# Performance work log

Measured on AMD Instinct MI355X. Metric: run time of the kernel, lower is better.

The kernel has to match this reference:

```python
import jax, jax.numpy as jnp
import numpy as np

B, N, HIDDEN, IN_DIM = 4, 1024, 64, 6


def setup_inputs() -> dict:
    key = jax.random.key(0)
    ks = jax.random.split(key, 8)
    pos = jax.random.normal(ks[0], (B, N, 3), dtype=jnp.float32)
    vel = jax.random.normal(ks[1], (B, N, 3), dtype=jnp.float32)
    # edge MLP params (Linear stores W as [out,in] in torch; we use [in,out])
    s1 = 1.0 / np.sqrt(IN_DIM)
    s2 = 1.0 / np.sqrt(HIDDEN)
    W1 = jax.random.uniform(ks[2], (IN_DIM, HIDDEN), jnp.float32, -s1, s1)
    b1 = jax.random.uniform(ks[3], (HIDDEN,), jnp.float32, -s1, s1)
    W2 = jax.random.uniform(ks[4], (HIDDEN, HIDDEN), jnp.float32, -s2, s2)
    b2 = jax.random.uniform(ks[5], (HIDDEN,), jnp.float32, -s2, s2)
    W3 = jax.random.uniform(ks[6], (HIDDEN, 3), jnp.float32, -s2, s2)
    b3 = jax.random.uniform(ks[7], (3,), jnp.float32, -s2, s2)
    return {"pos": pos, "vel": vel, "W1": W1, "b1": b1, "W2": W2, "b2": b2, "W3": W3, "b3": b3}


def reference(pos, vel, W1, b1, W2, b2, W3, b3):
    # all-pairs differences: r_ij[b,i,j] = pos[b,j] - pos[b,i]   [B,N,N,3]
    r_ij = pos[:, None, :, :] - pos[:, :, None, :]
    v_ij = vel[:, None, :, :] - vel[:, :, None, :]
    edge_inputs = jnp.concatenate([r_ij, v_ij], axis=-1)  # [B,N,N,6]
    h = jax.nn.relu(jnp.einsum('bijk,kh->bijh', edge_inputs, W1) + b1)
    h = jax.nn.relu(jnp.einsum('bijh,hg->bijg', h, W2) + b2)
    f_ij = jnp.einsum('bijg,go->bijo', h, W3) + b3  # [B,N,N,3]
    # antisymmetrize over (i,j); diagonal becomes exactly 0
    f_sym = (f_ij - jnp.swapaxes(f_ij, 1, 2)) * 0.5
    acc = jnp.sum(f_sym, axis=2)  # [B,N,3]
    return acc
```

## Files before the change

### kernel.cpp

```cpp
#include <hip/hip_runtime.h>

#define NB   4
#define NPTS 1024
#define HID  64
#define TPB  64
#define UPB  2080

typedef float f32x4 __attribute__((ext_vector_type(4)));
typedef float f32x2 __attribute__((ext_vector_type(2)));
typedef short bf16x8 __attribute__((ext_vector_type(8)));
typedef unsigned int u32;
typedef unsigned short u16;

__device__ inline u16 f2bf(float x) {
    union { float f; unsigned u; } v; v.f = x;
    return (u16)((v.u + 0x7FFFu + ((v.u >> 16) & 1u)) >> 16);
}
__device__ inline u32 cvt_pk_bf16(float lo, float hi) {
    u32 r; asm("v_cvt_pk_bf16_f32 %0, %1, %2" : "=v"(r) : "v"(lo), "v"(hi)); return r;
}
__device__ inline u32 pk_relu2(u32 a) {
    u32 r; asm("v_pk_max_i16 %0, %1, 0" : "=v"(r) : "v"(a)); return r;
}

__global__ __launch_bounds__(256) void precompute(
    const float* __restrict__ pos, const float* __restrict__ vel,
    const float* __restrict__ W1, const float* __restrict__ W2,
    float* __restrict__ P, u16* __restrict__ W2T) {
    if (blockIdx.x == NB * NPTS / 4) {
        for (int e = threadIdx.x; e < HID * HID; e += 256) {
            const int ch = e >> 6, k = e & 63;
            W2T[e] = f2bf(W2[k * HID + ch]);
        }
        return;
    }
    const int t   = blockIdx.x * 256 + threadIdx.x;
    const int row = t >> 6;
    const int k   = t & 63;
    const float* pp = pos + row * 3;
    const float* vv = vel + row * 3;
    float acc = 0.f;
    #pragma unroll
    for (int c = 0; c < 3; ++c) acc = fmaf(pp[c], W1[c * HID + k], acc);
    #pragma unroll
    for (int c = 0; c < 3; ++c) acc = fmaf(vv[c], W1[(3 + c) * HID + k], acc);
    P[row * HID + k] = acc;
}

__device__ inline void emit_tile(const f32x4 Ht[4], float sgn, int rowbase,
                                 const float* __restrict__ W3,
                                 float* __restrict__ F, int c, int g) {
    #pragma unroll
    for (int r = 0; r < 4; ++r) {
        float f0 = 0.f, f1 = 0.f, f2 = 0.f;
        #pragma unroll
        for (int n = 0; n < 4; ++n) {
            const int ch = n * 16 + c;
            const float h = Ht[n][r];
            f0 = fmaf(h, W3[ch * 3 + 0], f0);
            f1 = fmaf(h, W3[ch * 3 + 1], f1);
            f2 = fmaf(h, W3[ch * 3 + 2], f2);
        }
        #pragma unroll
        for (int off = 1; off < 16; off <<= 1) {
            f0 += __shfl_xor(f0, off, 64);
            f1 += __shfl_xor(f1, off, 64);
            f2 += __shfl_xor(f2, off, 64);
        }
        if (c < 3) {
            const float v = (c == 0) ? f0 : ((c == 1) ? f1 : f2);
            atomicAdd(&F[(size_t)(rowbase + g * 4 + r) * 3 + c], sgn * v);
        }
    }
}

__global__ __launch_bounds__(128, 3) void inet_pair(
    const float* __restrict__ P,  const float* __restrict__ b1,
    const u16* __restrict__ W2T,  const float* __restrict__ b2,
    const float* __restrict__ W3, float* __restrict__ F) {
    __shared__ __align__(16) u16 sBf[512 * 8];

    const int tid = threadIdx.x;
    for (int s = tid; s < 512; s += 128) {
        const int f = s >> 6, l = s & 63;
        const int n = f & 3, kk = f >> 2, cc = l & 15, gg = l >> 4;
        ((uint4*)sBf)[s] = *(const uint4*)(W2T + (size_t)(n * 16 + cc) * HID + kk * 32 + gg * 8);
    }
    __syncthreads();

    const int lane = tid & 63;
    const int c    = lane & 15;
    const int g    = lane >> 4;

    const int unit = blockIdx.x * 2 + (tid >> 6);
    const int b    = unit / UPB;
    const int p    = unit - b * UPB;
    int I = (int)((129.0f - sqrtf((float)(16641 - 8 * p))) * 0.5f);
    while (I * (129 - I) / 2 > p) --I;
    while ((I + 1) * (128 - I) / 2 <= p) ++I;
    const int J = I + (p - I * (129 - I) / 2);
    const bool diag = (I == J);

    const float* Pb   = P + (size_t)b * NPTS * HID;
    const int    koff = g * 8;

    union V4 { f32x4 v; f32x2 p[2]; };

    f32x2 PJp[8], PJm[8];
    {
        const float* base = Pb + (size_t)(J * 16 + c) * HID + koff;
        V4 v0, v1, v2, v3, u0, u1, u2, u3;
        v0.v = *(const f32x4*)(base);
        v1.v = *(const f32x4*)(base + 4);
        v2.v = *(const f32x4*)(base + 32);
        v3.v = *(const f32x4*)(base + 36);
        u0.v = *(const f32x4*)(b1 + koff);
        u1.v = *(const f32x4*)(b1 + koff + 4);
        u2.v = *(const f32x4*)(b1 + koff + 32);
        u3.v = *(const f32x4*)(b1 + koff + 36);
        PJp[0] = v0.p[0] + u0.p[0];  PJm[0] = v0.p[0] - u0.p[0];
        PJp[1] = v0.p[1] + u0.p[1];  PJm[1] = v0.p[1] - u0.p[1];
        PJp[2] = v1.p[0] + u1.p[0];  PJm[2] = v1.p[0] - u1.p[0];
        PJp[3] = v1.p[1] + u1.p[1];  PJm[3] = v1.p[1] - u1.p[1];
        PJp[4] = v2.p[0] + u2.p[0];  PJm[4] = v2.p[0] - u2.p[0];
        PJp[5] = v2.p[1] + u2.p[1];  PJm[5] = v2.p[1] - u2.p[1];
        PJp[6] = v3.p[0] + u3.p[0];  PJm[6] = v3.p[0] - u3.p[0];
        PJp[7] = v3.p[1] + u3.p[1];  PJm[7] = v3.p[1] - u3.p[1];
    }
    float b2v[4];
    #pragma unroll
    for (int n = 0; n < 4; ++n) b2v[n] = b2[n * 16 + c];

    f32x4 Hi[4], Hj[4];
    #pragma unroll
    for (int n = 0; n < 4; ++n) {
        Hi[n] = (f32x4){0.f, 0.f, 0.f, 0.f};
        Hj[n] = (f32x4){0.f, 0.f, 0.f, 0.f};
    }

    const float* Pi0 = Pb + (size_t)(I * 16) * HID + koff;

    for (int i1 = 0; i1 < 4; ++i1) {
        const float selm = (g == i1) ? 1.0f : 0.0f;
        #pragma unroll
        for (int i2 = 0; i2 < 4; ++i2) {
            const float* pib = Pi0 + (size_t)(i1 * 4 + i2) * HID;
            V4 w0, w1, w2, w3;
            w0.v = *(const f32x4*)(pib);
            w1.v = *(const f32x4*)(pib + 4);
            w2.v = *(const f32x4*)(pib + 32);
            w3.v = *(const f32x4*)(pib + 36);
            f32x2 pi2[8];
            pi2[0] = w0.p[0]; pi2[1] = w0.p[1]; pi2[2] = w1.p[0]; pi2[3] = w1.p[1];
            pi2[4] = w2.p[0]; pi2[5] = w2.p[1]; pi2[6] = w3.p[0]; pi2[7] = w3.p[1];

            union { bf16x8 v; u32 u[4]; } ap[2], am[2];
            #pragma unroll
            for (int kk = 0; kk < 2; ++kk)
                #pragma unroll
                for (int d = 0; d < 4; ++d) {
                    f32x2 tp = PJp[kk * 4 + d] - pi2[kk * 4 + d];
                    f32x2 tm = pi2[kk * 4 + d] - PJm[kk * 4 + d];
                    ap[kk].u[d] = pk_relu2(cvt_pk_bf16(tp.x, tp.y));
                    am[kk].u[d] = pk_relu2(cvt_pk_bf16(tm.x, tm.y));
                }

            #pragma unroll
            for (int n = 0; n < 4; ++n) {
                const bf16x8 B0 = ((const bf16x8*)sBf)[n * 64 + lane];
                const bf16x8 B1 = ((const bf16x8*)sBf)[(4 + n) * 64 + lane];
                const f32x4 Ci = {b2v[n], b2v[n], b2v[n], b2v[n]};
                f32x4 Cp = __builtin_amdgcn_mfma_f32_16x16x32_bf16(ap[0].v, B0, Ci, 0, 0, 0);
                Cp       = __builtin_amdgcn_mfma_f32_16x16x32_bf16(ap[1].v, B1, Cp, 0, 0, 0);
                f32x4 Cm = __builtin_amdgcn_mfma_f32_16x16x32_bf16(am[0].v, B0, Ci, 0, 0, 0);
                Cm       = __builtin_amdgcn_mfma_f32_16x16x32_bf16(am[1].v, B1, Cm, 0, 0, 0);
                V4 dd;
                dd.p[0] = (f32x2){fmaxf(Cp[0], 0.f) - fmaxf(Cm[0], 0.f),
                                  fmaxf(Cp[1], 0.f) - fmaxf(Cm[1], 0.f)};
                dd.p[1] = (f32x2){fmaxf(Cp[2], 0.f) - fmaxf(Cm[2], 0.f),
                                  fmaxf(Cp[3], 0.f) - fmaxf(Cm[3], 0.f)};
                if (!diag) {
                    Hj[n][0] += dd.v[0]; Hj[n][1] += dd.v[1];
                    Hj[n][2] += dd.v[2]; Hj[n][3] += dd.v[3];
                }
                f32x2 q = dd.p[0] + dd.p[1];
                float s = q.x + q.y;
                s += __shfl_xor(s, 16, 64);
                s += __shfl_xor(s, 32, 64);
                Hi[n][i2] = fmaf(selm, s, Hi[n][i2]);
            }
        }
    }

    const int rowbase = b * NPTS;
    emit_tile(Hi, 0.5f, rowbase + I * 16, W3, F, c, g);
    if (!diag)
        emit_tile(Hj, -0.5f, rowbase + J * 16, W3, F, c, g);
}

extern "C" void kernel_launch(void* const* d_in, const int* in_sizes, int n_in,
                              void* d_out, int out_size, void* d_ws, size_t ws_size,
                              hipStream_t stream) {
    const float* pos = (const float*)d_in[0];
    const float* vel = (const float*)d_in[1];
    const float* W1  = (const float*)d_in[2];
    const float* b1  = (const float*)d_in[3];
    const float* W2  = (const float*)d_in[4];
    const float* b2  = (const float*)d_in[5];
    const float* W3  = (const float*)d_in[6];
    const float* b3  = (const float*)d_in[7];
    (void)b3;
    float* out = (float*)d_out;
    float* P   = (float*)d_ws;
    u16*   W2T = (u16*)((char*)d_ws + (size_t)NB * NPTS * HID * 4);

    hipMemsetAsync(out, 0, (size_t)out_size * sizeof(float), stream);
    precompute<<<dim3(NB * NPTS / 4 + 1), dim3(256), 0, stream>>>(pos, vel, W1, W2, P, W2T);
    inet_pair<<<dim3(NB * UPB / 2), dim3(128), 0, stream>>>(P, b1, W2T, b2, W3, out);
}
```

Before: 112.8 us.

## Hold W2 fragments in registers and reduce i-side sums via LDS atomics

W2 bf16 MFMA fragments are now loaded straight into registers per wave instead of being staged through shared memory with a block barrier. The per-row i-side reduction, which used two cross-lane shuffles and a masked FMA per step, becomes an LDS atomicAdd into a per-wave 16x64 tile. The i-side epilogue is rewritten to read that tile and apply W3 with a 4-lane shuffle reduction. This removes shuffle work and the shared staging sync, at the cost of more registers (launch bound lowered from 3 to 2 waves per SIMD) and many LDS atomics.

```diff
diff --git a/kernel.cpp b/kernel.cpp
--- a/kernel.cpp
+++ b/kernel.cpp
@@ -74,25 +74,23 @@
     }
 }
 
-__global__ __launch_bounds__(128, 3) void inet_pair(
+__global__ __launch_bounds__(128, 2) void inet_pair(
     const float* __restrict__ P,  const float* __restrict__ b1,
     const u16* __restrict__ W2T,  const float* __restrict__ b2,
     const float* __restrict__ W3, float* __restrict__ F) {
-    __shared__ __align__(16) u16 sBf[512 * 8];
-
-    const int tid = threadIdx.x;
-    for (int s = tid; s < 512; s += 128) {
-        const int f = s >> 6, l = s & 63;
-        const int n = f & 3, kk = f >> 2, cc = l & 15, gg = l >> 4;
-        ((uint4*)sBf)[s] = *(const uint4*)(W2T + (size_t)(n * 16 + cc) * HID + kk * 32 + gg * 8);
-    }
-    __syncthreads();
-
+    __shared__ float sHi[2][16 * HID];
+
+    const int tid  = threadIdx.x;
+    const int wv   = tid >> 6;
     const int lane = tid & 63;
     const int c    = lane & 15;
     const int g    = lane >> 4;
 
-    const int unit = blockIdx.x * 2 + (tid >> 6);
+    #pragma unroll
+    for (int t = 0; t < 4; ++t)
+        ((f32x4*)sHi[wv])[lane * 4 + t] = (f32x4){0.f, 0.f, 0.f, 0.f};
+
+    const int unit = blockIdx.x * 2 + wv;
     const int b    = unit / UPB;
     const int p    = unit - b * UPB;
     int I = (int)((129.0f - sqrtf((float)(16641 - 8 * p))) * 0.5f);
@@ -105,6 +103,13 @@
     const int    koff = g * 8;
 
     union V4 { f32x4 v; f32x2 p[2]; };
+
+    bf16x8 Bf[8];
+    #pragma unroll
+    for (int kk = 0; kk < 2; ++kk)
+        #pragma unroll
+        for (int n = 0; n < 4; ++n)
+            Bf[kk * 4 + n] = *(const bf16x8*)(W2T + (size_t)(n * 16 + c) * HID + kk * 32 + g * 8);
 
     f32x2 PJp[8], PJm[8];
     {
@@ -131,17 +136,14 @@
     #pragma unroll
     for (int n = 0; n < 4; ++n) b2v[n] = b2[n * 16 + c];
 
-    f32x4 Hi[4], Hj[4];
-    #pragma unroll
-    for (int n = 0; n < 4; ++n) {
-        Hi[n] = (f32x4){0.f, 0.f, 0.f, 0.f};
-        Hj[n] = (f32x4){0.f, 0.f, 0.f, 0.f};
-    }
+    f32x4 Hj[4];
+    #pragma unroll
+    for (int n = 0; n < 4; ++n) Hj[n] = (f32x4){0.f, 0.f, 0.f, 0.f};
 
     const float* Pi0 = Pb + (size_t)(I * 16) * HID + koff;
+    float* sH = sHi[wv];
 
     for (int i1 = 0; i1 < 4; ++i1) {
-        const float selm = (g == i1) ? 1.0f : 0.0f;
         #pragma unroll
         for (int i2 = 0; i2 < 4; ++i2) {
             const float* pib = Pi0 + (size_t)(i1 * 4 + i2) * HID;
@@ -167,13 +169,11 @@
 
             #pragma unroll
             for (int n = 0; n < 4; ++n) {
-                const bf16x8 B0 = ((const bf16x8*)sBf)[n * 64 + lane];
-                const bf16x8 B1 = ((const bf16x8*)sBf)[(4 + n) * 64 + lane];
                 const f32x4 Ci = {b2v[n], b2v[n], b2v[n], b2v[n]};
-                f32x4 Cp = __builtin_amdgcn_mfma_f32_16x16x32_bf16(ap[0].v, B0, Ci, 0, 0, 0);
-                Cp       = __builtin_amdgcn_mfma_f32_16x16x32_bf16(ap[1].v, B1, Cp, 0, 0, 0);
-                f32x4 Cm = __builtin_amdgcn_mfma_f32_16x16x32_bf16(am[0].v, B0, Ci, 0, 0, 0);
-                Cm       = __builtin_amdgcn_mfma_f32_16x16x32_bf16(am[1].v, B1, Cm, 0, 0, 0);
+                f32x4 Cp = __builtin_amdgcn_mfma_f32_16x16x32_bf16(ap[0].v, Bf[n],     Ci, 0, 0, 0);
+                Cp       = __builtin_amdgcn_mfma_f32_16x16x32_bf16(ap[1].v, Bf[4 + n], Cp, 0, 0, 0);
+                f32x4 Cm = __builtin_amdgcn_mfma_f32_16x16x32_bf16(am[0].v, Bf[n],     Ci, 0, 0, 0);
+                Cm       = __builtin_amdgcn_mfma_f32_16x16x32_bf16(am[1].v, Bf[4 + n], Cm, 0, 0, 0);
                 V4 dd;
                 dd.p[0] = (f32x2){fmaxf(Cp[0], 0.f) - fmaxf(Cm[0], 0.f),
                                   fmaxf(Cp[1], 0.f) - fmaxf(Cm[1], 0.f)};
@@ -184,16 +184,50 @@
                     Hj[n][2] += dd.v[2]; Hj[n][3] += dd.v[3];
                 }
                 f32x2 q = dd.p[0] + dd.p[1];
-                float s = q.x + q.y;
-                s += __shfl_xor(s, 16, 64);
-                s += __shfl_xor(s, 32, 64);
-                Hi[n][i2] = fmaf(selm, s, Hi[n][i2]);
+                atomicAdd(&sH[(i1 * 4 + i2) * HID + n * 16 + c], q.x + q.y);
             }
         }
     }
 
     const int rowbase = b * NPTS;
-    emit_tile(Hi, 0.5f, rowbase + I * 16, W3, F, c, g);
+
+    asm volatile("s_waitcnt lgkmcnt(0)" ::: "memory");
+    {
+        const int li = lane >> 2, q = lane & 3;
+        const float* hrow = sH + li * HID + q * 16;
+        f32x4 h0 = ((const f32x4*)hrow)[0];
+        f32x4 h1 = ((const f32x4*)hrow)[1];
+        f32x4 h2 = ((const f32x4*)hrow)[2];
+        f32x4 h3 = ((const f32x4*)hrow)[3];
+        float hv[16];
+        #pragma unroll
+        for (int e = 0; e < 4; ++e) {
+            hv[e] = h0[e]; hv[4 + e] = h1[e]; hv[8 + e] = h2[e]; hv[12 + e] = h3[e];
+        }
+        const float* w3q = W3 + q * 48;
+        float wq[48];
+        #pragma unroll
+        for (int t = 0; t < 12; ++t) {
+            f32x4 wv4 = ((const f32x4*)w3q)[t];
+            wq[t * 4 + 0] = wv4[0]; wq[t * 4 + 1] = wv4[1];
+            wq[t * 4 + 2] = wv4[2]; wq[t * 4 + 3] = wv4[3];
+        }
+        float f0 = 0.f, f1 = 0.f, f2 = 0.f;
+        #pragma unroll
+        for (int e = 0; e < 16; ++e) {
+            f0 = fmaf(hv[e], wq[e * 3 + 0], f0);
+            f1 = fmaf(hv[e], wq[e * 3 + 1], f1);
+            f2 = fmaf(hv[e], wq[e * 3 + 2], f2);
+        }
+        f0 += __shfl_xor(f0, 1, 64);  f0 += __shfl_xor(f0, 2, 64);
+        f1 += __shfl_xor(f1, 1, 64);  f1 += __shfl_xor(f1, 2, 64);
+        f2 += __shfl_xor(f2, 1, 64);  f2 += __shfl_xor(f2, 2, 64);
+        if (q < 3) {
+            const float v = (q == 0) ? f0 : ((q == 1) ? f1 : f2);
+            atomicAdd(&F[(size_t)(rowbase + I * 16 + li) * 3 + q], 0.5f * v);
+        }
+    }
+
     if (!diag)
         emit_tile(Hj, -0.5f, rowbase + J * 16, W3, F, c, g);
 }
```

Measured after the change: 207.3 us. 83.7% more time.
